# Kernel tuning notes

Measured on AMD Instinct MI355X. Metric: run time of the kernel, lower is better.

Reference implementation:

```python
import jax, jax.numpy as jnp
import numpy as np

NUM_HEADS = 8


def setup_inputs() -> dict:
    key = jax.random.key(0)
    k1, k2 = jax.random.split(key)
    B, N, C = 2, 8192, 512
    x = jax.random.normal(k1, (B, N, C), dtype=jnp.float32)
    # torch nn.Linear weight layout: [out_features, in_features]
    W_qkv = jax.random.normal(k2, (3 * C, C), dtype=jnp.float32) * (C ** -0.5)
    return {"x": x, "W_qkv": W_qkv}


def reference(x, W_qkv):
    B, N, C = x.shape
    H = NUM_HEADS
    d = C // H
    scale = d ** -0.5

    # qkv projection (no bias): [B, N, 3C]
    qkv = x @ W_qkv.T
    # [B, N, 3, H, d] -> [3, B, H, N, d]
    qkv = qkv.reshape(B, N, 3, H, d).transpose(2, 0, 3, 1, 4)
    q, k, v = qkv[0], qkv[1], qkv[2]

    # mean-center keys over sequence dim
    k_hat = k - jnp.mean(k, axis=2, keepdims=True)          # [B, H, N, d]

    # KV aggregation: g = k_hat^T @ v  -> [B, H, d, d]
    g = jnp.einsum('bhnd,bhne->bhde', k_hat, v)

    # k_sum over sequence (numerically ~0 since k_hat is centered, kept faithful)
    k_sum = jnp.sum(k_hat, axis=2)                          # [B, H, d]
    q_ksum = jnp.einsum('bhnd,bhd->bhn', q, k_sum)[..., None]  # [B, H, N, 1]

    # denominator: N*scale + q @ k_sum^T
    t_D = N * scale + q_ksum                                # [B, H, N, 1]
    # numerator: scale + q @ g (broadcast of ones*scale over last dim)
    T_N = scale + jnp.einsum('bhnd,bhde->bhne', q, g)       # [B, H, N, d]

    z = T_N / t_D                                           # [B, H, N, d]
    return z
```

## Files before the change

kernel.cpp:

```cpp
#include <hip/hip_runtime.h>

typedef unsigned short u16;
typedef unsigned int u32;
typedef __attribute__((ext_vector_type(8))) short short8;
typedef __attribute__((ext_vector_type(4))) float f32x4;
typedef __attribute__((ext_vector_type(4))) unsigned short ushort4v;
typedef __attribute__((ext_vector_type(4))) float float4v;

__device__ __forceinline__ float bf2f(u16 u) {
    return __uint_as_float(((u32)u) << 16);
}
__device__ __forceinline__ u16 f2bf(float f) {
    u32 u = __float_as_uint(f);
    u += 0x7FFF + ((u >> 16) & 1);
    return (u16)(u >> 16);
}

__global__ __launch_bounds__(256) void cvt_bf16(const float* __restrict__ in,
                                                u16* __restrict__ out, int n4) {
    int i = blockIdx.x * 256 + threadIdx.x;
    int stride = gridDim.x * 256;
    for (; i < n4; i += stride) {
        float4v v = ((const float4v*)in)[i];
        ushort4v r;
        r[0] = f2bf(v[0]); r[1] = f2bf(v[1]); r[2] = f2bf(v[2]); r[3] = f2bf(v[3]);
        ((ushort4v*)out)[i] = r;
    }
}

__global__ __launch_bounds__(256) void gemm_qkv(const u16* __restrict__ xb,
                                                const u16* __restrict__ wb,
                                                u16* __restrict__ qkv) {
    __shared__ u16 As[128 * 32];
    __shared__ u16 Bs[128 * 32];
    const int t = threadIdx.x;
    const int m0 = blockIdx.x * 128;
    const int n0 = blockIdx.y * 128;
    const int l = t & 63, w = t >> 6;
    const int wm = (w >> 1) * 64, wn = (w & 1) * 64;
    const int lr = l & 15, lk = (l >> 4) * 8;
    const int sr = t >> 2, sc = (t & 3) * 8;
    const u16* ag = xb + (size_t)(m0 + sr) * 512 + sc;
    const u16* bg = wb + (size_t)(n0 + sr) * 512 + sc;

    f32x4 zz = {0.f, 0.f, 0.f, 0.f};
    f32x4 acc[4][4];
    for (int i = 0; i < 4; ++i)
        for (int j = 0; j < 4; ++j) acc[i][j] = zz;

    for (int k0 = 0; k0 < 512; k0 += 32) {
        int4 a0 = *(const int4*)(ag + k0);
        int4 a1 = *(const int4*)(ag + 64 * 512 + k0);
        int4 b0 = *(const int4*)(bg + k0);
        int4 b1 = *(const int4*)(bg + 64 * 512 + k0);
        __syncthreads();
        *(int4*)(As + sr * 32 + sc) = a0;
        *(int4*)(As + (sr + 64) * 32 + sc) = a1;
        *(int4*)(Bs + sr * 32 + sc) = b0;
        *(int4*)(Bs + (sr + 64) * 32 + sc) = b1;
        __syncthreads();
        short8 af[4], bfr[4];
#pragma unroll
        for (int mi = 0; mi < 4; ++mi)
            af[mi] = *(const short8*)(As + (wm + mi * 16 + lr) * 32 + lk);
#pragma unroll
        for (int ni = 0; ni < 4; ++ni)
            bfr[ni] = *(const short8*)(Bs + (wn + ni * 16 + lr) * 32 + lk);
#pragma unroll
        for (int mi = 0; mi < 4; ++mi)
#pragma unroll
            for (int ni = 0; ni < 4; ++ni)
                acc[mi][ni] = __builtin_amdgcn_mfma_f32_16x16x32_bf16(
                    af[mi], bfr[ni], acc[mi][ni], 0, 0, 0);
    }
#pragma unroll
    for (int mi = 0; mi < 4; ++mi)
#pragma unroll
        for (int ni = 0; ni < 4; ++ni) {
            int col = n0 + wn + ni * 16 + lr;
#pragma unroll
            for (int j = 0; j < 4; ++j) {
                int row = m0 + wm + mi * 16 + (l >> 4) * 4 + j;
                qkv[(size_t)row * 1536 + col] = f2bf(acc[mi][ni][j]);
            }
        }
}

__global__ __launch_bounds__(256) void kv_outer(const u16* __restrict__ qkv,
                                                float* __restrict__ gpart,
                                                float* __restrict__ ksump,
                                                float* __restrict__ vsump) {
    const int bh = blockIdx.x >> 5, s = blockIdx.x & 31;
    const int b = bh >> 3, h = bh & 7;
    const int t = threadIdx.x;
    const int tx = t & 15, ty = t >> 4;
    __shared__ u16 ks[64 * 64];
    __shared__ u16 vs[64 * 64];
    const u16* kg = qkv + ((size_t)(b * 8192 + s * 256)) * 1536 + 512 + h * 64;
    const u16* vg = kg + 512;
    const int sr = t >> 3, sc = (t & 7) * 8;

    float acc[4][4];
    for (int i = 0; i < 4; ++i)
        for (int j = 0; j < 4; ++j) acc[i][j] = 0.f;
    float ka[4] = {0.f, 0.f, 0.f, 0.f}, va[4] = {0.f, 0.f, 0.f, 0.f};

    for (int c = 0; c < 4; ++c) {
        const u16* kgc = kg + (size_t)(c * 64 + sr) * 1536 + sc;
        const u16* vgc = vg + (size_t)(c * 64 + sr) * 1536 + sc;
        int4 k0v = *(const int4*)kgc;
        int4 k1v = *(const int4*)(kgc + (size_t)32 * 1536);
        int4 v0v = *(const int4*)vgc;
        int4 v1v = *(const int4*)(vgc + (size_t)32 * 1536);
        __syncthreads();
        *(int4*)(ks + sr * 64 + sc) = k0v;
        *(int4*)(ks + (sr + 32) * 64 + sc) = k1v;
        *(int4*)(vs + sr * 64 + sc) = v0v;
        *(int4*)(vs + (sr + 32) * 64 + sc) = v1v;
        __syncthreads();
#pragma unroll 4
        for (int n = 0; n < 64; ++n) {
            ushort4v k4 = *(const ushort4v*)(ks + n * 64 + ty * 4);
            ushort4v v4 = *(const ushort4v*)(vs + n * 64 + tx * 4);
            float kf[4], vf[4];
#pragma unroll
            for (int i = 0; i < 4; ++i) { kf[i] = bf2f(k4[i]); vf[i] = bf2f(v4[i]); }
#pragma unroll
            for (int i = 0; i < 4; ++i)
#pragma unroll
                for (int j = 0; j < 4; ++j) acc[i][j] += kf[i] * vf[j];
#pragma unroll
            for (int i = 0; i < 4; ++i) { ka[i] += kf[i]; va[i] += vf[i]; }
        }
    }
    size_t gb = ((size_t)(bh * 32 + s)) * 4096;
#pragma unroll
    for (int i = 0; i < 4; ++i)
#pragma unroll
        for (int j = 0; j < 4; ++j)
            gpart[gb + (ty * 4 + i) * 64 + tx * 4 + j] = acc[i][j];
    if (tx == 0)
        for (int i = 0; i < 4; ++i) ksump[(bh * 32 + s) * 64 + ty * 4 + i] = ka[i];
    if (ty == 0)
        for (int i = 0; i < 4; ++i) vsump[(bh * 32 + s) * 64 + tx * 4 + i] = va[i];
}

__global__ __launch_bounds__(256) void g_final(const float* __restrict__ gpart,
                                               const float* __restrict__ ksump,
                                               const float* __restrict__ vsump,
                                               u16* __restrict__ gt) {
    const int bh = blockIdx.x >> 4, part = blockIdx.x & 15;
    const int t = threadIdx.x;
    __shared__ float kls[64], vls[64];
    if (t < 64) {
        float s = 0.f;
        for (int j = 0; j < 32; ++j) s += ksump[(bh * 32 + j) * 64 + t];
        kls[t] = s;
    } else if (t < 128) {
        int d = t - 64;
        float s = 0.f;
        for (int j = 0; j < 32; ++j) s += vsump[(bh * 32 + j) * 64 + d];
        vls[d] = s;
    }
    __syncthreads();
    const int idx = part * 256 + t;
    const int d1 = idx >> 6, d2 = idx & 63;
    float s = 0.f;
    for (int j = 0; j < 32; ++j) s += gpart[((size_t)(bh * 32 + j)) * 4096 + idx];
    s -= kls[d1] * vls[d2] * (1.0f / 8192.0f);
    gt[bh * 4096 + d2 * 64 + d1] = f2bf(s);
}

__global__ __launch_bounds__(256) void out_z(const u16* __restrict__ qkv,
                                             const u16* __restrict__ gt,
                                             float* __restrict__ z) {
    const int bh = blockIdx.x >> 6, chunk = blockIdx.x & 63;
    const int b = bh >> 3, h = bh & 7;
    const int t = threadIdx.x, l = t & 63, w = t >> 6;
    const int lr = l & 15, lk = (l >> 4) * 8;
    const u16* qcol = qkv + ((size_t)b * 8192) * 1536 + h * 64;
    const u16* gb = gt + bh * 4096;

    short8 bfr[2][4];
#pragma unroll
    for (int kk = 0; kk < 2; ++kk)
#pragma unroll
        for (int ni = 0; ni < 4; ++ni)
            bfr[kk][ni] = *(const short8*)(gb + (ni * 16 + lr) * 64 + kk * 32 + lk);

    f32x4 zz = {0.f, 0.f, 0.f, 0.f};
    f32x4 acc[2][4];
    for (int i = 0; i < 2; ++i)
        for (int j = 0; j < 4; ++j) acc[i][j] = zz;

    const int r0 = chunk * 128 + w * 32;
#pragma unroll
    for (int kk = 0; kk < 2; ++kk)
#pragma unroll
        for (int mi = 0; mi < 2; ++mi) {
            short8 af = *(const short8*)(qcol + (size_t)(r0 + mi * 16 + lr) * 1536 + kk * 32 + lk);
#pragma unroll
            for (int ni = 0; ni < 4; ++ni)
                acc[mi][ni] = __builtin_amdgcn_mfma_f32_16x16x32_bf16(
                    af, bfr[kk][ni], acc[mi][ni], 0, 0, 0);
        }

    const float sc = 0.125f;
    const float inv = 1.0f / 1024.0f;
#pragma unroll
    for (int mi = 0; mi < 2; ++mi)
#pragma unroll
        for (int ni = 0; ni < 4; ++ni) {
            int col = ni * 16 + lr;
#pragma unroll
            for (int j = 0; j < 4; ++j) {
                int row = r0 + mi * 16 + (l >> 4) * 4 + j;
                z[((size_t)bh * 8192 + row) * 64 + col] = (sc + acc[mi][ni][j]) * inv;
            }
        }
}

extern "C" void kernel_launch(void* const* d_in, const int* in_sizes, int n_in,
                              void* d_out, int out_size, void* d_ws, size_t ws_size,
                              hipStream_t stream) {
    const float* x = (const float*)d_in[0];
    const float* W = (const float*)d_in[1];
    float* z = (float*)d_out;

    char* ws = (char*)d_ws;
    u16* xb    = (u16*)(ws);
    u16* wb    = (u16*)(ws + 16777216);
    u16* qkv   = (u16*)(ws + 18350080);
    float* gpart = (float*)(ws + 68681728);
    float* ksump = (float*)(ws + 77070336);
    float* vsump = (float*)(ws + 77201408);
    u16* gt    = (u16*)(ws + 77332480);

    cvt_bf16<<<2048, 256, 0, stream>>>(x, xb, 8388608 / 4);
    cvt_bf16<<<384, 256, 0, stream>>>(W, wb, 786432 / 4);
    gemm_qkv<<<dim3(128, 12), 256, 0, stream>>>(xb, wb, qkv);
    kv_outer<<<512, 256, 0, stream>>>(qkv, gpart, ksump, vsump);
    g_final<<<256, 256, 0, stream>>>(gpart, ksump, vsump, gt);
    out_z<<<1024, 256, 0, stream>>>(qkv, gt, z);
}
```

Before: 96.07 us.

## Fold Q projection into per-head G matrix and skip materializing Q

Instead of computing Q in the QKV GEMM and then multiplying Q by G, the kernel now computes only K and V, then folds W_q^T·G into a per-batch weight matrix (fold kernel) and computes z directly as x·(W_q G) in a second full GEMM. The GEMM staging switches to direct global-to-LDS loads via global_load_lds. The aim is to avoid writing and rereading the Q third of the projection and to turn the small per-head output product into a well-shaped GEMM. In exchange it adds a fold kernel, a larger output GEMM over K=512 instead of 64, and extra bf16 rounding of the folded weights.

```diff
diff --git a/kernel.cpp b/kernel.cpp
--- a/kernel.cpp
+++ b/kernel.cpp
@@ -14,6 +14,12 @@
     u32 u = __float_as_uint(f);
     u += 0x7FFF + ((u >> 16) & 1);
     return (u16)(u >> 16);
+}
+
+__device__ __forceinline__ void stage16(const u16* g, u16* l) {
+    __builtin_amdgcn_global_load_lds(
+        (const __attribute__((address_space(1))) unsigned int*)g,
+        (__attribute__((address_space(3))) unsigned int*)l, 16, 0, 0);
 }
 
 __global__ __launch_bounds__(256) void cvt_bf16(const float* __restrict__ in,
@@ -28,36 +34,29 @@
     }
 }
 
-__global__ __launch_bounds__(256) void gemm_qkv(const u16* __restrict__ xb,
-                                                const u16* __restrict__ wb,
-                                                u16* __restrict__ qkv) {
-    __shared__ u16 As[128 * 32];
-    __shared__ u16 Bs[128 * 32];
-    const int t = threadIdx.x;
-    const int m0 = blockIdx.x * 128;
-    const int n0 = blockIdx.y * 128;
-    const int l = t & 63, w = t >> 6;
-    const int wm = (w >> 1) * 64, wn = (w & 1) * 64;
+__device__ __forceinline__ void gemm_core(const u16* __restrict__ Ag,
+                                          const u16* __restrict__ Bg,
+                                          u16* As, u16* Bs, int t,
+                                          f32x4 acc[4][4]) {
+    const int wv = t >> 6, l = t & 63;
     const int lr = l & 15, lk = (l >> 4) * 8;
-    const int sr = t >> 2, sc = (t & 3) * 8;
-    const u16* ag = xb + (size_t)(m0 + sr) * 512 + sc;
-    const u16* bg = wb + (size_t)(n0 + sr) * 512 + sc;
-
-    f32x4 zz = {0.f, 0.f, 0.f, 0.f};
-    f32x4 acc[4][4];
-    for (int i = 0; i < 4; ++i)
-        for (int j = 0; j < 4; ++j) acc[i][j] = zz;
+    const int wm = (wv >> 1) * 64, wn = (wv & 1) * 64;
+    const int srow = l >> 2, scol = (l & 3) * 8;
+
+    u16* Ad0 = As + (wv * 32) * 32;
+    u16* Ad1 = As + (wv * 32 + 16) * 32;
+    u16* Bd0 = Bs + (wv * 32) * 32;
+    u16* Bd1 = Bs + (wv * 32 + 16) * 32;
+    const u16* As0 = Ag + (size_t)(wv * 32 + srow) * 512 + scol;
+    const u16* As1 = Ag + (size_t)(wv * 32 + 16 + srow) * 512 + scol;
+    const u16* Bs0 = Bg + (size_t)(wv * 32 + srow) * 512 + scol;
+    const u16* Bs1 = Bg + (size_t)(wv * 32 + 16 + srow) * 512 + scol;
 
     for (int k0 = 0; k0 < 512; k0 += 32) {
-        int4 a0 = *(const int4*)(ag + k0);
-        int4 a1 = *(const int4*)(ag + 64 * 512 + k0);
-        int4 b0 = *(const int4*)(bg + k0);
-        int4 b1 = *(const int4*)(bg + 64 * 512 + k0);
-        __syncthreads();
-        *(int4*)(As + sr * 32 + sc) = a0;
-        *(int4*)(As + (sr + 64) * 32 + sc) = a1;
-        *(int4*)(Bs + sr * 32 + sc) = b0;
-        *(int4*)(Bs + (sr + 64) * 32 + sc) = b1;
+        stage16(As0 + k0, Ad0);
+        stage16(As1 + k0, Ad1);
+        stage16(Bs0 + k0, Bd0);
+        stage16(Bs1 + k0, Bd1);
         __syncthreads();
         short8 af[4], bfr[4];
 #pragma unroll
@@ -72,7 +71,28 @@
             for (int ni = 0; ni < 4; ++ni)
                 acc[mi][ni] = __builtin_amdgcn_mfma_f32_16x16x32_bf16(
                     af[mi], bfr[ni], acc[mi][ni], 0, 0, 0);
-    }
+        __syncthreads();
+    }
+}
+
+__global__ __launch_bounds__(256) void gemm_kv(const u16* __restrict__ xb,
+                                               const u16* __restrict__ wb,
+                                               u16* __restrict__ kvb) {
+    __shared__ u16 As[128 * 32];
+    __shared__ u16 Bs[128 * 32];
+    const int t = threadIdx.x;
+    const int m0 = blockIdx.x * 128;
+    const int n0 = blockIdx.y * 128;
+    f32x4 zz = {0.f, 0.f, 0.f, 0.f};
+    f32x4 acc[4][4];
+    for (int i = 0; i < 4; ++i)
+        for (int j = 0; j < 4; ++j) acc[i][j] = zz;
+
+    gemm_core(xb + (size_t)m0 * 512, wb + (size_t)n0 * 512, As, Bs, t, acc);
+
+    const int l = t & 63, wv = t >> 6;
+    const int lr = l & 15;
+    const int wm = (wv >> 1) * 64, wn = (wv & 1) * 64;
 #pragma unroll
     for (int mi = 0; mi < 4; ++mi)
 #pragma unroll
@@ -81,12 +101,12 @@
 #pragma unroll
             for (int j = 0; j < 4; ++j) {
                 int row = m0 + wm + mi * 16 + (l >> 4) * 4 + j;
-                qkv[(size_t)row * 1536 + col] = f2bf(acc[mi][ni][j]);
+                kvb[(size_t)row * 1024 + col] = f2bf(acc[mi][ni][j]);
             }
         }
 }
 
-__global__ __launch_bounds__(256) void kv_outer(const u16* __restrict__ qkv,
+__global__ __launch_bounds__(256) void kv_outer(const u16* __restrict__ kvb,
                                                 float* __restrict__ gpart,
                                                 float* __restrict__ ksump,
                                                 float* __restrict__ vsump) {
@@ -96,7 +116,7 @@
     const int tx = t & 15, ty = t >> 4;
     __shared__ u16 ks[64 * 64];
     __shared__ u16 vs[64 * 64];
-    const u16* kg = qkv + ((size_t)(b * 8192 + s * 256)) * 1536 + 512 + h * 64;
+    const u16* kg = kvb + ((size_t)(b * 8192 + s * 256)) * 1024 + h * 64;
     const u16* vg = kg + 512;
     const int sr = t >> 3, sc = (t & 7) * 8;
 
@@ -106,12 +126,12 @@
     float ka[4] = {0.f, 0.f, 0.f, 0.f}, va[4] = {0.f, 0.f, 0.f, 0.f};
 
     for (int c = 0; c < 4; ++c) {
-        const u16* kgc = kg + (size_t)(c * 64 + sr) * 1536 + sc;
-        const u16* vgc = vg + (size_t)(c * 64 + sr) * 1536 + sc;
+        const u16* kgc = kg + (size_t)(c * 64 + sr) * 1024 + sc;
+        const u16* vgc = vg + (size_t)(c * 64 + sr) * 1024 + sc;
         int4 k0v = *(const int4*)kgc;
-        int4 k1v = *(const int4*)(kgc + (size_t)32 * 1536);
+        int4 k1v = *(const int4*)(kgc + (size_t)32 * 1024);
         int4 v0v = *(const int4*)vgc;
-        int4 v1v = *(const int4*)(vgc + (size_t)32 * 1536);
+        int4 v1v = *(const int4*)(vgc + (size_t)32 * 1024);
         __syncthreads();
         *(int4*)(ks + sr * 64 + sc) = k0v;
         *(int4*)(ks + (sr + 32) * 64 + sc) = k1v;
@@ -148,7 +168,7 @@
 __global__ __launch_bounds__(256) void g_final(const float* __restrict__ gpart,
                                                const float* __restrict__ ksump,
                                                const float* __restrict__ vsump,
-                                               u16* __restrict__ gt) {
+                                               float* __restrict__ gfull) {
     const int bh = blockIdx.x >> 4, part = blockIdx.x & 15;
     const int t = threadIdx.x;
     __shared__ float kls[64], vls[64];
@@ -168,54 +188,66 @@
     float s = 0.f;
     for (int j = 0; j < 32; ++j) s += gpart[((size_t)(bh * 32 + j)) * 4096 + idx];
     s -= kls[d1] * vls[d2] * (1.0f / 8192.0f);
-    gt[bh * 4096 + d2 * 64 + d1] = f2bf(s);
-}
-
-__global__ __launch_bounds__(256) void out_z(const u16* __restrict__ qkv,
-                                             const u16* __restrict__ gt,
+    gfull[bh * 4096 + idx] = s;
+}
+
+__global__ __launch_bounds__(256) void fold(const float* __restrict__ gfull,
+                                            const float* __restrict__ W,
+                                            u16* __restrict__ Wgb) {
+    const int bh = blockIdx.x >> 3, cb = blockIdx.x & 7;
+    const int b = bh >> 3, h = bh & 7;
+    const int t = threadIdx.x;
+    __shared__ float gs[4096];
+    for (int i = t; i < 4096; i += 256) gs[i] = gfull[bh * 4096 + i];
+    __syncthreads();
+    const int c = cb * 64 + (t & 63);
+    const int eg = (t >> 6) * 16;
+    float acc[16];
+#pragma unroll
+    for (int j = 0; j < 16; ++j) acc[j] = 0.f;
+    for (int d = 0; d < 64; ++d) {
+        float w = W[(size_t)(h * 64 + d) * 512 + c];
+#pragma unroll
+        for (int j = 0; j < 16; ++j) acc[j] += w * gs[d * 64 + eg + j];
+    }
+#pragma unroll
+    for (int j = 0; j < 16; ++j)
+        Wgb[(size_t)(b * 512 + h * 64 + eg + j) * 512 + c] = f2bf(acc[j]);
+}
+
+__global__ __launch_bounds__(256) void out_z(const u16* __restrict__ xb,
+                                             const u16* __restrict__ Wgb,
                                              float* __restrict__ z) {
-    const int bh = blockIdx.x >> 6, chunk = blockIdx.x & 63;
-    const int b = bh >> 3, h = bh & 7;
-    const int t = threadIdx.x, l = t & 63, w = t >> 6;
-    const int lr = l & 15, lk = (l >> 4) * 8;
-    const u16* qcol = qkv + ((size_t)b * 8192) * 1536 + h * 64;
-    const u16* gb = gt + bh * 4096;
-
-    short8 bfr[2][4];
-#pragma unroll
-    for (int kk = 0; kk < 2; ++kk)
-#pragma unroll
-        for (int ni = 0; ni < 4; ++ni)
-            bfr[kk][ni] = *(const short8*)(gb + (ni * 16 + lr) * 64 + kk * 32 + lk);
+    __shared__ u16 As[128 * 32];
+    __shared__ u16 Bs[128 * 32];
+    const int t = threadIdx.x;
+    const int m0 = blockIdx.x * 128;
+    const int b = blockIdx.x >> 6;
+    const int n0 = blockIdx.y * 128;
 
     f32x4 zz = {0.f, 0.f, 0.f, 0.f};
-    f32x4 acc[2][4];
-    for (int i = 0; i < 2; ++i)
+    f32x4 acc[4][4];
+    for (int i = 0; i < 4; ++i)
         for (int j = 0; j < 4; ++j) acc[i][j] = zz;
 
-    const int r0 = chunk * 128 + w * 32;
-#pragma unroll
-    for (int kk = 0; kk < 2; ++kk)
-#pragma unroll
-        for (int mi = 0; mi < 2; ++mi) {
-            short8 af = *(const short8*)(qcol + (size_t)(r0 + mi * 16 + lr) * 1536 + kk * 32 + lk);
-#pragma unroll
-            for (int ni = 0; ni < 4; ++ni)
-                acc[mi][ni] = __builtin_amdgcn_mfma_f32_16x16x32_bf16(
-                    af, bfr[kk][ni], acc[mi][ni], 0, 0, 0);
-        }
-
-    const float sc = 0.125f;
-    const float inv = 1.0f / 1024.0f;
-#pragma unroll
-    for (int mi = 0; mi < 2; ++mi)
+    gemm_core(xb + (size_t)m0 * 512,
+              Wgb + (size_t)b * 262144 + (size_t)n0 * 512, As, Bs, t, acc);
+
+    const int l = t & 63, wv = t >> 6;
+    const int lr = l & 15;
+    const int wm = (wv >> 1) * 64, wn = (wv & 1) * 64;
+#pragma unroll
+    for (int mi = 0; mi < 4; ++mi)
 #pragma unroll
         for (int ni = 0; ni < 4; ++ni) {
-            int col = ni * 16 + lr;
+            int he = n0 + wn + ni * 16 + lr;
+            int h = he >> 6, e = he & 63;
 #pragma unroll
             for (int j = 0; j < 4; ++j) {
-                int row = r0 + mi * 16 + (l >> 4) * 4 + j;
-                z[((size_t)bh * 8192 + row) * 64 + col] = (sc + acc[mi][ni][j]) * inv;
+                int row = m0 + wm + mi * 16 + (l >> 4) * 4 + j;
+                int nidx = row & 8191;
+                z[((size_t)(b * 8 + h) * 8192 + nidx) * 64 + e] =
+                    (acc[mi][ni][j] + 0.125f) * 0.0009765625f;
             }
         }
 }
@@ -228,18 +260,20 @@
     float* z = (float*)d_out;
 
     char* ws = (char*)d_ws;
-    u16* xb    = (u16*)(ws);
-    u16* wb    = (u16*)(ws + 16777216);
-    u16* qkv   = (u16*)(ws + 18350080);
-    float* gpart = (float*)(ws + 68681728);
-    float* ksump = (float*)(ws + 77070336);
-    float* vsump = (float*)(ws + 77201408);
-    u16* gt    = (u16*)(ws + 77332480);
+    u16* xb      = (u16*)(ws);
+    u16* wb      = (u16*)(ws + 16777216);
+    u16* kvb     = (u16*)(ws + 17825792);
+    float* gpart = (float*)(ws + 51380224);
+    float* ksump = (float*)(ws + 59768832);
+    float* vsump = (float*)(ws + 59899904);
+    float* gfull = (float*)(ws + 60030976);
+    u16* Wgb     = (u16*)(ws + 60293120);
 
     cvt_bf16<<<2048, 256, 0, stream>>>(x, xb, 8388608 / 4);
-    cvt_bf16<<<384, 256, 0, stream>>>(W, wb, 786432 / 4);
-    gemm_qkv<<<dim3(128, 12), 256, 0, stream>>>(xb, wb, qkv);
-    kv_outer<<<512, 256, 0, stream>>>(qkv, gpart, ksump, vsump);
-    g_final<<<256, 256, 0, stream>>>(gpart, ksump, vsump, gt);
-    out_z<<<1024, 256, 0, stream>>>(qkv, gt, z);
-}
+    cvt_bf16<<<512, 256, 0, stream>>>(W + 262144, wb, 524288 / 4);
+    gemm_kv<<<dim3(128, 8), 256, 0, stream>>>(xb, wb, kvb);
+    kv_outer<<<512, 256, 0, stream>>>(kvb, gpart, ksump, vsump);
+    g_final<<<256, 256, 0, stream>>>(gpart, ksump, vsump, gfull);
+    fold<<<128, 256, 0, stream>>>(gfull, W, Wgb);
+    out_z<<<dim3(128, 4), 256, 0, stream>>>(xb, Wgb, z);
+}
```

Result: slower. 100.9 us (+5.1%).
